# Optimization experiments

Measured on AMD Instinct MI355X. Metric: run time of the kernel, lower is better.

The kernel has to match this reference:

```python
import jax, jax.numpy as jnp
import numpy as np

N = 50000      # nodes
E = 800000     # edges (avg degree 16)
F_IN = 128     # input feature dim
HID = 64       # hidden_channels
HEADS = 4
OUT = 64       # out_channels


def _gatv2_layer(x, src, dst, Wl, Wr, att, bias, heads, ch, n):
    # lin_l (source) and lin_r (target) projections -> [N, H, C]
    xl = (x @ Wl).reshape(n, heads, ch)
    xr = (x @ Wr).reshape(n, heads, ch)
    # per-edge GATv2 attention logits: a^T LeakyReLU(xl_j + xr_i)
    e = jax.nn.leaky_relu(xl[src] + xr[dst], negative_slope=0.2)  # [E, H, C]
    score = jnp.einsum('ehc,hc->eh', e, att)                      # [E, H]
    # segment softmax over incoming edges of each destination node
    m = jax.ops.segment_max(score, dst, num_segments=n)           # [N, H]
    m = jnp.where(jnp.isfinite(m), m, 0.0)
    p = jnp.exp(score - m[dst])
    denom = jax.ops.segment_sum(p, dst, num_segments=n)           # [N, H]
    alpha = p / (denom[dst] + 1e-16)                              # [E, H]
    # weighted scatter-aggregate of source messages xl_j
    out = jax.ops.segment_sum(alpha[..., None] * xl[src], dst, num_segments=n)
    return out.reshape(n, heads * ch) + bias


def setup_inputs() -> dict:
    key = jax.random.key(0)
    ks = jax.random.split(key, 16)

    def w(k, shape, fan_in):
        return (jax.random.normal(k, shape, dtype=jnp.float32) / np.sqrt(fan_in)).astype(jnp.float32)

    return {
        'x': jax.random.normal(ks[0], (N, F_IN), dtype=jnp.float32),
        'Wl1': w(ks[1], (F_IN, HEADS * HID), F_IN),
        'Wr1': w(ks[2], (F_IN, HEADS * HID), F_IN),
        'att1': w(ks[3], (HEADS, HID), HID),
        'b1': jnp.zeros((HEADS * HID,), jnp.float32),
        'Wl2': w(ks[4], (HEADS * HID, HEADS * HID), HEADS * HID),
        'Wr2': w(ks[5], (HEADS * HID, HEADS * HID), HEADS * HID),
        'att2': w(ks[6], (HEADS, HID), HID),
        'b2': jnp.zeros((HEADS * HID,), jnp.float32),
        'Wl3': w(ks[7], (HEADS * HID, OUT), HEADS * HID),
        'Wr3': w(ks[8], (HEADS * HID, OUT), HEADS * HID),
        'att3': w(ks[9], (1, OUT), OUT),
        'b3': jnp.zeros((OUT,), jnp.float32),
        'Wlin': w(ks[10], (OUT, HID), OUT),
        'blin': jnp.zeros((HID,), jnp.float32),
        'edge_index': jax.random.randint(ks[11], (2, E), 0, N, dtype=jnp.int64
                                         if jax.config.read('jax_enable_x64') else jnp.int32),
    }


def reference(x, Wl1, Wr1, att1, b1, Wl2, Wr2, att2, b2, Wl3, Wr3, att3, b3, Wlin, blin, edge_index):
    src, dst = edge_index[0], edge_index[1]
    h = jax.nn.elu(_gatv2_layer(x, src, dst, Wl1, Wr1, att1, b1, HEADS, HID, N))
    h = jax.nn.elu(_gatv2_layer(h, src, dst, Wl2, Wr2, att2, b2, HEADS, HID, N))
    h = _gatv2_layer(h, src, dst, Wl3, Wr3, att3, b3, 1, OUT, N)
    # F.dropout(p=0.5, training=False) -> identity in eval mode
    return h @ Wlin + blin
```

## Files before the change

kernel.cpp:

```cpp
#include <hip/hip_runtime.h>
#include <hip/hip_fp16.h>

#define NN 50000
#define EE 800000

typedef float f32x4 __attribute__((ext_vector_type(4)));
typedef _Float16 f16x8 __attribute__((ext_vector_type(8)));
typedef _Float16 f16x4 __attribute__((ext_vector_type(4)));
typedef _Float16 f16x2 __attribute__((ext_vector_type(2)));

__global__ void hist_kernel(const int* __restrict__ dst, int* __restrict__ counts, int E) {
    int idx = blockIdx.x * blockDim.x + threadIdx.x;
    int stride = gridDim.x * blockDim.x;
    for (int e = idx; e < E; e += stride)
        atomicAdd(&counts[dst[e]], 1);
}

__global__ void scan_phaseA(const int* __restrict__ counts, int* __restrict__ bsum, int n) {
    __shared__ int buf[256];
    int b = blockIdx.x, t = threadIdx.x;
    int i = b * 256 + t;
    buf[t] = (i < n) ? counts[i] : 0;
    __syncthreads();
#pragma unroll
    for (int off = 128; off; off >>= 1) {
        if (t < off) buf[t] += buf[t + off];
        __syncthreads();
    }
    if (t == 0) bsum[b] = buf[0];
}

__global__ void scan_phaseB(int* __restrict__ bsum, int* __restrict__ row_off_n, int nb) {
    __shared__ int buf[256];
    int t = threadIdx.x;
    int v = (t < nb) ? bsum[t] : 0;
    buf[t] = v;
    __syncthreads();
#pragma unroll
    for (int off = 1; off < 256; off <<= 1) {
        int x = (t >= off) ? buf[t - off] : 0;
        __syncthreads();
        buf[t] += x;
        __syncthreads();
    }
    if (t < nb) bsum[t] = buf[t] - v;
    if (t == 255) *row_off_n = buf[255];
}

__global__ void scan_phaseC(const int* __restrict__ counts, const int* __restrict__ bsum,
                            int* __restrict__ row_off, int n) {
    __shared__ int buf[256];
    int b = blockIdx.x, t = threadIdx.x;
    int i = b * 256 + t;
    int v = (i < n) ? counts[i] : 0;
    buf[t] = v;
    __syncthreads();
#pragma unroll
    for (int off = 1; off < 256; off <<= 1) {
        int x = (t >= off) ? buf[t - off] : 0;
        __syncthreads();
        buf[t] += x;
        __syncthreads();
    }
    if (i < n) row_off[i] = bsum[b] + buf[t] - v;
}

__global__ void scatter_kernel(const int* __restrict__ src, const int* __restrict__ dst,
                               const int* __restrict__ row_off, int* __restrict__ cursor,
                               int* __restrict__ esrc, int E) {
    int idx = blockIdx.x * blockDim.x + threadIdx.x;
    int stride = gridDim.x * blockDim.x;
    for (int e = idx; e < E; e += stride) {
        int d = dst[e];
        int pos = row_off[d] + atomicAdd(&cursor[d], 1);
        esrc[pos] = src[e];
    }
}

__device__ __forceinline__ void wfrag_store(__half* o, int K, int col, int k, float v) {
    int KS = K >> 5;
    int cgni = col >> 4, l15 = col & 15;
    int ks = k >> 5, qq = (k >> 3) & 3, ee = k & 7;
    size_t flat = ((size_t)(cgni * KS + ks) * 64 + qq * 16 + l15) * 8 + ee;
    o[flat] = __float2half_rn(v);
}

__global__ void prep_all(const float* __restrict__ Wl1, const float* __restrict__ Wr1,
                         const float* __restrict__ Wl2, const float* __restrict__ Wr2,
                         const float* __restrict__ Wl3, const float* __restrict__ Wr3,
                         const float* __restrict__ Wlin,
                         __half* __restrict__ w1, __half* __restrict__ w2,
                         __half* __restrict__ w3, __half* __restrict__ w4,
                         const float* __restrict__ x, __half* __restrict__ xf, int n4x) {
    int idx = blockIdx.x * blockDim.x + threadIdx.x;
    if (idx < 233472) {
        const float* W; __half* o; int K, Nc, roff, li;
        if (idx < 65536) {
            K = 128; Nc = 256; o = w1;
            if (idx < 32768) { W = Wl1; li = idx; roff = 0; }
            else             { W = Wr1; li = idx - 32768; roff = 256; }
        } else if (idx < 196608) {
            K = 256; Nc = 256; o = w2;
            if (idx < 131072) { W = Wl2; li = idx - 65536; roff = 0; }
            else              { W = Wr2; li = idx - 131072; roff = 256; }
        } else if (idx < 229376) {
            K = 256; Nc = 64; o = w3;
            if (idx < 212992) { W = Wl3; li = idx - 196608; roff = 0; }
            else              { W = Wr3; li = idx - 212992; roff = 64; }
        } else {
            K = 64; Nc = 64; o = w4; W = Wlin; li = idx - 229376; roff = 0;
        }
        int k = li / Nc, n = li - k * Nc;
        wfrag_store(o, K, roff + n, k, W[li]);
    } else {
        int xi = idx - 233472;
        if (xi < n4x) {
            float4 v = *(const float4*)(x + (size_t)xi * 4);
            f16x4 h = {(_Float16)v.x, (_Float16)v.y, (_Float16)v.z, (_Float16)v.w};
            *(f16x4*)((_Float16*)xf + (size_t)xi * 4) = h;
        }
    }
}

template <int KS, int COLG>
__global__ __launch_bounds__(COLG * 256) void gemm_ws(
        const __half* __restrict__ A, const __half* __restrict__ Bt,
        int M, int nTiles, int Nc, int splitCol,
        __half* __restrict__ outL, __half* __restrict__ outR,
        float* __restrict__ outF, const float* __restrict__ bias) {
    constexpr int K = KS * 32;
    int tid = threadIdx.x;
    int lane = tid & 63;
    int w = tid >> 6;
    int rs = w & 3;
    int cg = w >> 2;
    int l15 = lane & 15, q = lane >> 4;
    int colbase = blockIdx.y * (COLG * 64) + cg * 64;

    const _Float16* Ap = (const _Float16*)A;
    const f16x8* Bf = (const f16x8*)Bt;
    int cgni0 = (blockIdx.y * COLG + cg) * 4;

    f16x8 bfrag[KS][4];
#pragma unroll
    for (int ks = 0; ks < KS; ++ks)
#pragma unroll
        for (int ni = 0; ni < 4; ++ni)
            bfrag[ks][ni] = Bf[((size_t)(cgni0 + ni) * KS + ks) * 64 + lane];

    int tile = blockIdx.x;
    if (tile >= nTiles) return;

    f16x8 afrag[KS];
    {
        int row = tile * 64 + rs * 16 + l15;
        if (row >= M) row = M - 1;
        const _Float16* ap = Ap + (size_t)row * K + q * 8;
#pragma unroll
        for (int ks = 0; ks < KS; ++ks) afrag[ks] = *(const f16x8*)(ap + ks * 32);
    }

    while (true) {
        int next = tile + gridDim.x;
        bool has = (next < nTiles);
        f16x8 anext[KS];
        if (has) {
            int row = next * 64 + rs * 16 + l15;
            if (row >= M) row = M - 1;
            const _Float16* ap = Ap + (size_t)row * K + q * 8;
#pragma unroll
            for (int ks = 0; ks < KS; ++ks) anext[ks] = *(const f16x8*)(ap + ks * 32);
        }

        f32x4 acc[4] = {};
#pragma unroll
        for (int ks = 0; ks < KS; ++ks)
#pragma unroll
            for (int ni = 0; ni < 4; ++ni)
                acc[ni] = __builtin_amdgcn_mfma_f32_16x16x32_f16(afrag[ks], bfrag[ks][ni], acc[ni], 0, 0, 0);

#pragma unroll
        for (int ni = 0; ni < 4; ++ni) {
            int gc = colbase + ni * 16 + l15;
            if (outF) {
                float bv = bias ? bias[gc] : 0.f;
#pragma unroll
                for (int r = 0; r < 4; ++r) {
                    int gr = tile * 64 + rs * 16 + q * 4 + r;
                    if (gr < M) outF[(size_t)gr * Nc + gc] = acc[ni][r] + bv;
                }
            } else {
                __half* dp = outL; int cc = gc;
                if (gc >= splitCol) { dp = outR; cc = gc - splitCol; }
#pragma unroll
                for (int r = 0; r < 4; ++r) {
                    int gr = tile * 64 + rs * 16 + q * 4 + r;
                    if (gr < M) dp[(size_t)gr * splitCol + cc] = __float2half_rn(acc[ni][r]);
                }
            }
        }
        if (!has) break;
#pragma unroll
        for (int ks = 0; ks < KS; ++ks) afrag[ks] = anext[ks];
        tile = next;
    }
}

template <int CTRL>
__device__ __forceinline__ float dpp_add_f32(float x) {
    int y = __builtin_amdgcn_mov_dpp(__float_as_int(x), CTRL, 0xF, 0xF, true);
    return x + __int_as_float(y);
}

__global__ __launch_bounds__(256, 4) void gat_gather_h4(
        const __half* __restrict__ xl, const __half* __restrict__ xr,
        const float* __restrict__ att, const float* __restrict__ bias,
        const int* __restrict__ row_off, const int* __restrict__ esrc,
        __half* __restrict__ out, int n) {
    const float LOG2E = 1.44269504f;
    int wave = threadIdx.x >> 6;
    int lane = threadIdx.x & 63;
    int node = blockIdx.x * 4 + wave;
    if (node >= n) return;
    int eslot = lane >> 4;
    unsigned j = lane & 15;

    const uint4* xl16 = (const uint4*)xl;
    unsigned jo = 2u * j;

    f16x2 xrv[8];
    *(uint4*)(&xrv[0]) = ((const uint4*)xr)[((unsigned)node << 5) + jo];
    *(uint4*)(&xrv[4]) = ((const uint4*)xr)[((unsigned)node << 5) + jo + 1];

    float4 a0 = *(const float4*)(att + j * 16);
    float4 a1 = *(const float4*)(att + j * 16 + 4);
    float4 a2 = *(const float4*)(att + j * 16 + 8);
    float4 a3 = *(const float4*)(att + j * 16 + 12);
    f16x2 atv[8] = {
        {(_Float16)(a0.x * LOG2E), (_Float16)(a0.y * LOG2E)},
        {(_Float16)(a0.z * LOG2E), (_Float16)(a0.w * LOG2E)},
        {(_Float16)(a1.x * LOG2E), (_Float16)(a1.y * LOG2E)},
        {(_Float16)(a1.z * LOG2E), (_Float16)(a1.w * LOG2E)},
        {(_Float16)(a2.x * LOG2E), (_Float16)(a2.y * LOG2E)},
        {(_Float16)(a2.z * LOG2E), (_Float16)(a2.w * LOG2E)},
        {(_Float16)(a3.x * LOG2E), (_Float16)(a3.y * LOG2E)},
        {(_Float16)(a3.z * LOG2E), (_Float16)(a3.w * LOG2E)}};
    const f16x2 k02 = {(_Float16)0.2f, (_Float16)0.2f};

    float acc[16] = {};
    float L = 0.f;

    int e0 = row_off[node], e1 = row_off[node + 1];
    int elast = (e1 > e0) ? e1 - 1 : 0;

    int sA = esrc[min(e0 + 0 + eslot, elast)];
    int sB = esrc[min(e0 + 4 + eslot, elast)];
    int sC = esrc[min(e0 + 8 + eslot, elast)];
    uint4 A0 = xl16[((unsigned)sA << 5) + jo], A1 = xl16[((unsigned)sA << 5) + jo + 1];
    uint4 B0 = xl16[((unsigned)sB << 5) + jo], B1 = xl16[((unsigned)sB << 5) + jo + 1];
    uint4 C0 = xl16[((unsigned)sC << 5) + jo], C1 = xl16[((unsigned)sC << 5) + jo + 1];

#define H4_PHASE(R0, R1, EB)                                                  \
    {                                                                         \
        f16x2 v[8];                                                           \
        *(uint4*)(&v[0]) = R0;                                                \
        *(uint4*)(&v[4]) = R1;                                                \
        float t0 = 0.f, t1 = 0.f;                                             \
        _Pragma("unroll")                                                     \
        for (int k = 0; k < 4; ++k) {                                         \
            f16x2 sa = v[k] + xrv[k];                                         \
            f16x2 ra = __builtin_elementwise_max(sa, sa * k02);               \
            t0 = __builtin_amdgcn_fdot2(ra, atv[k], t0, false);               \
            f16x2 sb = v[k + 4] + xrv[k + 4];                                 \
            f16x2 rb = __builtin_elementwise_max(sb, sb * k02);               \
            t1 = __builtin_amdgcn_fdot2(rb, atv[k + 4], t1, false);           \
        }                                                                     \
        float t = t0 + t1;                                                    \
        t = dpp_add_f32<0xB1>(t);                                             \
        t = dpp_add_f32<0x4E>(t);                                             \
        float p = exp2f(t);                                                   \
        p = ((EB) + eslot < e1) ? p : 0.f;                                    \
        L += p;                                                               \
        _Pragma("unroll")                                                     \
        for (int k = 0; k < 8; ++k) {                                         \
            acc[2 * k]     = fmaf((float)v[k].x, p, acc[2 * k]);              \
            acc[2 * k + 1] = fmaf((float)v[k].y, p, acc[2 * k + 1]);          \
        }                                                                     \
    }

    for (int e = e0; e < e1; e += 12) {
        int nsA = esrc[min(e + 12 + eslot, elast)];
        int nsB = esrc[min(e + 16 + eslot, elast)];
        int nsC = esrc[min(e + 20 + eslot, elast)];
        H4_PHASE(A0, A1, e)
        A0 = xl16[((unsigned)nsA << 5) + jo];
        A1 = xl16[((unsigned)nsA << 5) + jo + 1];
        H4_PHASE(B0, B1, e + 4)
        B0 = xl16[((unsigned)nsB << 5) + jo];
        B1 = xl16[((unsigned)nsB << 5) + jo + 1];
        H4_PHASE(C0, C1, e + 8)
        C0 = xl16[((unsigned)nsC << 5) + jo];
        C1 = xl16[((unsigned)nsC << 5) + jo + 1];
    }
#undef H4_PHASE

#pragma unroll
    for (int k = 0; k < 16; ++k) {
        acc[k] += __shfl_xor(acc[k], 16);
        acc[k] += __shfl_xor(acc[k], 32);
    }
    L += __shfl_xor(L, 16);
    L += __shfl_xor(L, 32);

    if (eslot == 0) {
        float inv = 1.f / (L + 1e-16f);
        float4 b0 = *(const float4*)(bias + j * 16);
        float4 b1v = *(const float4*)(bias + j * 16 + 4);
        float4 b2v = *(const float4*)(bias + j * 16 + 8);
        float4 b3v = *(const float4*)(bias + j * 16 + 12);
        float bb[16] = {b0.x,  b0.y,  b0.z,  b0.w,  b1v.x, b1v.y, b1v.z, b1v.w,
                        b2v.x, b2v.y, b2v.z, b2v.w, b3v.x, b3v.y, b3v.z, b3v.w};
        f16x8 o0, o1;
#pragma unroll
        for (int k = 0; k < 8; ++k) {
            float vA = acc[k] * inv + bb[k];
            vA = vA > 0.f ? vA : __expf(vA) - 1.f;
            o0[k] = (_Float16)vA;
            float vB = acc[k + 8] * inv + bb[k + 8];
            vB = vB > 0.f ? vB : __expf(vB) - 1.f;
            o1[k] = (_Float16)vB;
        }
        _Float16* op = (_Float16*)out + ((size_t)node << 8) + j * 16;
        *(f16x8*)op = o0;
        *(f16x8*)(op + 8) = o1;
    }
}

__global__ __launch_bounds__(256, 4) void gat_gather_h1(
        const __half* __restrict__ xl, const __half* __restrict__ xr,
        const float* __restrict__ att, const float* __restrict__ bias,
        const int* __restrict__ row_off, const int* __restrict__ esrc,
        __half* __restrict__ out, int n) {
    const float LOG2E = 1.44269504f;
    int wave = threadIdx.x >> 6;
    int lane = threadIdx.x & 63;
    int node = blockIdx.x * 4 + wave;
    if (node >= n) return;
    int eslot = lane >> 3;
    unsigned j = lane & 7;

    const uint4* xl16 = (const uint4*)xl;

    f16x2 xrv[4];
    *(uint4*)(&xrv[0]) = ((const uint4*)xr)[((unsigned)node << 3) + j];

    float4 a0 = *(const float4*)(att + j * 8);
    float4 a1 = *(const float4*)(att + j * 8 + 4);
    f16x2 atv[4] = {
        {(_Float16)(a0.x * LOG2E), (_Float16)(a0.y * LOG2E)},
        {(_Float16)(a0.z * LOG2E), (_Float16)(a0.w * LOG2E)},
        {(_Float16)(a1.x * LOG2E), (_Float16)(a1.y * LOG2E)},
        {(_Float16)(a1.z * LOG2E), (_Float16)(a1.w * LOG2E)}};
    const f16x2 k02 = {(_Float16)0.2f, (_Float16)0.2f};

    float acc[8] = {};
    float L = 0.f;

    int e0 = row_off[node], e1 = row_off[node + 1];
    int elast = (e1 > e0) ? e1 - 1 : 0;

    int sA = esrc[min(e0 +  0 + eslot, elast)];
    int sB = esrc[min(e0 +  8 + eslot, elast)];
    int sC = esrc[min(e0 + 16 + eslot, elast)];
    uint4 A = xl16[((unsigned)sA << 3) + j];
    uint4 B = xl16[((unsigned)sB << 3) + j];
    uint4 C = xl16[((unsigned)sC << 3) + j];

#define H1_PHASE(R, EB)                                                       \
    {                                                                         \
        f16x2 v[4];                                                           \
        *(uint4*)(&v[0]) = R;                                                 \
        float t0 = 0.f, t1 = 0.f;                                             \
        {                                                                     \
            f16x2 s0 = v[0] + xrv[0];                                         \
            f16x2 r0 = __builtin_elementwise_max(s0, s0 * k02);               \
            t0 = __builtin_amdgcn_fdot2(r0, atv[0], t0, false);               \
            f16x2 s1 = v[1] + xrv[1];                                         \
            f16x2 r1 = __builtin_elementwise_max(s1, s1 * k02);               \
            t0 = __builtin_amdgcn_fdot2(r1, atv[1], t0, false);               \
            f16x2 s2 = v[2] + xrv[2];                                         \
            f16x2 r2 = __builtin_elementwise_max(s2, s2 * k02);               \
            t1 = __builtin_amdgcn_fdot2(r2, atv[2], t1, false);               \
            f16x2 s3 = v[3] + xrv[3];                                         \
            f16x2 r3 = __builtin_elementwise_max(s3, s3 * k02);               \
            t1 = __builtin_amdgcn_fdot2(r3, atv[3], t1, false);               \
        }                                                                     \
        float t = t0 + t1;                                                    \
        t = dpp_add_f32<0xB1>(t);                                             \
        t = dpp_add_f32<0x4E>(t);                                             \
        t = dpp_add_f32<0x141>(t);                                            \
        float p = exp2f(t);                                                   \
        p = ((EB) + eslot < e1) ? p : 0.f;                                    \
        L += p;                                                               \
        _Pragma("unroll")                                                     \
        for (int k = 0; k < 4; ++k) {                                         \
            acc[2 * k]     = fmaf((float)v[k].x, p, acc[2 * k]);              \
            acc[2 * k + 1] = fmaf((float)v[k].y, p, acc[2 * k + 1]);          \
        }                                                                     \
    }

    for (int e = e0; e < e1; e += 24) {
        int nsA = esrc[min(e + 24 + eslot, elast)];
        int nsB = esrc[min(e + 32 + eslot, elast)];
        int nsC = esrc[min(e + 40 + eslot, elast)];
        H1_PHASE(A, e)
        A = xl16[((unsigned)nsA << 3) + j];
        H1_PHASE(B, e + 8)
        B = xl16[((unsigned)nsB << 3) + j];
        H1_PHASE(C, e + 16)
        C = xl16[((unsigned)nsC << 3) + j];
    }
#undef H1_PHASE

#pragma unroll
    for (int k = 0; k < 8; ++k) {
        acc[k] += __shfl_xor(acc[k], 8);
        acc[k] += __shfl_xor(acc[k], 16);
        acc[k] += __shfl_xor(acc[k], 32);
    }
    L += __shfl_xor(L, 8);
    L += __shfl_xor(L, 16);
    L += __shfl_xor(L, 32);

    if (eslot == 0) {
        float inv = 1.f / (L + 1e-16f);
        float4 b0 = *(const float4*)(bias + j * 8);
        float4 b1v = *(const float4*)(bias + j * 8 + 4);
        float bb[8] = {b0.x, b0.y, b0.z, b0.w, b1v.x, b1v.y, b1v.z, b1v.w};
        f16x8 ov;
#pragma unroll
        for (int k = 0; k < 8; ++k)
            ov[k] = (_Float16)(acc[k] * inv + bb[k]);
        *(f16x8*)((_Float16*)out + ((size_t)node << 6) + j * 8) = ov;
    }
}

extern "C" void kernel_launch(void* const* d_in, const int* in_sizes, int n_in,
                              void* d_out, int out_size, void* d_ws, size_t ws_size,
                              hipStream_t stream) {
    const float* x    = (const float*)d_in[0];
    const float* Wl1  = (const float*)d_in[1];
    const float* Wr1  = (const float*)d_in[2];
    const float* att1 = (const float*)d_in[3];
    const float* b1   = (const float*)d_in[4];
    const float* Wl2  = (const float*)d_in[5];
    const float* Wr2  = (const float*)d_in[6];
    const float* att2 = (const float*)d_in[7];
    const float* b2   = (const float*)d_in[8];
    const float* Wl3  = (const float*)d_in[9];
    const float* Wr3  = (const float*)d_in[10];
    const float* att3 = (const float*)d_in[11];
    const float* b3   = (const float*)d_in[12];
    const float* Wlin = (const float*)d_in[13];
    const float* blin = (const float*)d_in[14];
    const int*   ei   = (const int*)d_in[15];
    const int* src = ei;
    const int* dst = ei + EE;

    const int N = NN, E = EE;
    const int NB = (N + 255) / 256;

    __half* xf = (__half*)d_ws;
    __half* xl = xf + (size_t)N * 128;
    __half* xr = xl + (size_t)N * 256;
    __half* H  = xr + (size_t)N * 256;
    __half* G  = H + (size_t)N * 256;
    __half* w1 = G + (size_t)N * 64;
    __half* w2 = w1 + 65536;
    __half* w3 = w2 + 131072;
    __half* w4 = w3 + 32768;
    int* row_off = (int*)(w4 + 4096);
    int* tmp     = row_off + (N + 1);
    int* esrc    = tmp + 2 * N;
    int* bsum    = esrc + E;

    hipMemsetAsync(tmp, 0, (size_t)2 * N * sizeof(int), stream);
    hist_kernel<<<1024, 256, 0, stream>>>(dst, tmp, E);
    scan_phaseA<<<NB, 256, 0, stream>>>(tmp, bsum, N);
    scan_phaseB<<<1, 256, 0, stream>>>(bsum, row_off + N, NB);
    scan_phaseC<<<NB, 256, 0, stream>>>(tmp, bsum, row_off, N);
    scatter_kernel<<<1024, 256, 0, stream>>>(src, dst, row_off, tmp + N, esrc, E);

    int n4x = N * 128 / 4;
    prep_all<<<(233472 + n4x + 255) / 256, 256, 0, stream>>>(
        Wl1, Wr1, Wl2, Wr2, Wl3, Wr3, Wlin, w1, w2, w3, w4, x, xf, n4x);

    int nTiles = (N + 63) / 64;
    int gatherBlocks = (N + 3) / 4;

    gemm_ws<4, 2><<<dim3(128, 4), 512, 0, stream>>>(
        xf, w1, N, nTiles, 512, 256, xl, xr, nullptr, nullptr);
    gat_gather_h4<<<gatherBlocks, 256, 0, stream>>>(xl, xr, att1, b1, row_off, esrc, H, N);

    gemm_ws<8, 2><<<dim3(128, 4), 512, 0, stream>>>(
        H, w2, N, nTiles, 512, 256, xl, xr, nullptr, nullptr);
    gat_gather_h4<<<gatherBlocks, 256, 0, stream>>>(xl, xr, att2, b2, row_off, esrc, H, N);

    gemm_ws<8, 2><<<dim3(256, 1), 512, 0, stream>>>(
        H, w3, N, nTiles, 128, 64, xl, xr, nullptr, nullptr);
    gat_gather_h1<<<gatherBlocks, 256, 0, stream>>>(xl, xr, att3, b3, row_off, esrc, G, N);

    gemm_ws<2, 1><<<dim3(512, 1), 256, 0, stream>>>(
        G, w4, N, nTiles, 64, 64, nullptr, nullptr, (float*)d_out, blin);
}
```

Baseline: 477.5 us.

## Remap 4-head gather to 32 lanes per edge with finer-grained early-exit loops

The 4-head gather kernel now gives each edge 32 lanes holding 8 channels each, processing 2 edges per wave step instead of 4 edges with 16 channels per lane. This halves the per-lane accumulator and register footprint, and the launch bound is raised to 8 blocks per CU to allow more resident waves. Both gather kernels switch from fixed multi-phase iterations to loops that exit after each phase, cutting masked wasted work on low-degree nodes. The trade-offs are an extra DPP reduction step per edge and more serial phases per node.

```diff
diff --git a/kernel.cpp b/kernel.cpp
--- a/kernel.cpp
+++ b/kernel.cpp
@@ -212,7 +212,7 @@
     return x + __int_as_float(y);
 }
 
-__global__ __launch_bounds__(256, 4) void gat_gather_h4(
+__global__ __launch_bounds__(256, 8) void gat_gather_h4(
         const __half* __restrict__ xl, const __half* __restrict__ xr,
         const float* __restrict__ att, const float* __restrict__ bias,
         const int* __restrict__ row_off, const int* __restrict__ esrc,
@@ -222,121 +222,106 @@
     int lane = threadIdx.x & 63;
     int node = blockIdx.x * 4 + wave;
     if (node >= n) return;
-    int eslot = lane >> 4;
-    unsigned j = lane & 15;
+    int slot = lane >> 5;
+    unsigned jj = lane & 31;
 
     const uint4* xl16 = (const uint4*)xl;
-    unsigned jo = 2u * j;
-
-    f16x2 xrv[8];
-    *(uint4*)(&xrv[0]) = ((const uint4*)xr)[((unsigned)node << 5) + jo];
-    *(uint4*)(&xrv[4]) = ((const uint4*)xr)[((unsigned)node << 5) + jo + 1];
-
-    float4 a0 = *(const float4*)(att + j * 16);
-    float4 a1 = *(const float4*)(att + j * 16 + 4);
-    float4 a2 = *(const float4*)(att + j * 16 + 8);
-    float4 a3 = *(const float4*)(att + j * 16 + 12);
-    f16x2 atv[8] = {
+
+    f16x2 xrv[4];
+    *(uint4*)(&xrv[0]) = ((const uint4*)xr)[((unsigned)node << 5) + jj];
+
+    float4 a0 = *(const float4*)(att + jj * 8);
+    float4 a1 = *(const float4*)(att + jj * 8 + 4);
+    f16x2 atv[4] = {
         {(_Float16)(a0.x * LOG2E), (_Float16)(a0.y * LOG2E)},
         {(_Float16)(a0.z * LOG2E), (_Float16)(a0.w * LOG2E)},
         {(_Float16)(a1.x * LOG2E), (_Float16)(a1.y * LOG2E)},
-        {(_Float16)(a1.z * LOG2E), (_Float16)(a1.w * LOG2E)},
-        {(_Float16)(a2.x * LOG2E), (_Float16)(a2.y * LOG2E)},
-        {(_Float16)(a2.z * LOG2E), (_Float16)(a2.w * LOG2E)},
-        {(_Float16)(a3.x * LOG2E), (_Float16)(a3.y * LOG2E)},
-        {(_Float16)(a3.z * LOG2E), (_Float16)(a3.w * LOG2E)}};
+        {(_Float16)(a1.z * LOG2E), (_Float16)(a1.w * LOG2E)}};
     const f16x2 k02 = {(_Float16)0.2f, (_Float16)0.2f};
 
-    float acc[16] = {};
+    float acc[8] = {};
     float L = 0.f;
 
     int e0 = row_off[node], e1 = row_off[node + 1];
     int elast = (e1 > e0) ? e1 - 1 : 0;
 
-    int sA = esrc[min(e0 + 0 + eslot, elast)];
-    int sB = esrc[min(e0 + 4 + eslot, elast)];
-    int sC = esrc[min(e0 + 8 + eslot, elast)];
-    uint4 A0 = xl16[((unsigned)sA << 5) + jo], A1 = xl16[((unsigned)sA << 5) + jo + 1];
-    uint4 B0 = xl16[((unsigned)sB << 5) + jo], B1 = xl16[((unsigned)sB << 5) + jo + 1];
-    uint4 C0 = xl16[((unsigned)sC << 5) + jo], C1 = xl16[((unsigned)sC << 5) + jo + 1];
-
-#define H4_PHASE(R0, R1, EB)                                                  \
+    int sA = esrc[min(e0 + 0 + slot, elast)];
+    int sB = esrc[min(e0 + 2 + slot, elast)];
+    int sC = esrc[min(e0 + 4 + slot, elast)];
+    int sD = esrc[min(e0 + 6 + slot, elast)];
+    uint4 A = xl16[((unsigned)sA << 5) + jj];
+    uint4 B = xl16[((unsigned)sB << 5) + jj];
+    uint4 C = xl16[((unsigned)sC << 5) + jj];
+    uint4 D = xl16[((unsigned)sD << 5) + jj];
+
+#define H4_PHASE(BUF, EB)                                                     \
     {                                                                         \
-        f16x2 v[8];                                                           \
-        *(uint4*)(&v[0]) = R0;                                                \
-        *(uint4*)(&v[4]) = R1;                                                \
-        float t0 = 0.f, t1 = 0.f;                                             \
+        f16x2 v[4];                                                           \
+        *(uint4*)(&v[0]) = BUF;                                               \
+        float t = 0.f;                                                        \
         _Pragma("unroll")                                                     \
         for (int k = 0; k < 4; ++k) {                                         \
-            f16x2 sa = v[k] + xrv[k];                                         \
-            f16x2 ra = __builtin_elementwise_max(sa, sa * k02);               \
-            t0 = __builtin_amdgcn_fdot2(ra, atv[k], t0, false);               \
-            f16x2 sb = v[k + 4] + xrv[k + 4];                                 \
-            f16x2 rb = __builtin_elementwise_max(sb, sb * k02);               \
-            t1 = __builtin_amdgcn_fdot2(rb, atv[k + 4], t1, false);           \
+            f16x2 s = v[k] + xrv[k];                                          \
+            f16x2 r = __builtin_elementwise_max(s, s * k02);                  \
+            t = __builtin_amdgcn_fdot2(r, atv[k], t, false);                  \
         }                                                                     \
-        float t = t0 + t1;                                                    \
         t = dpp_add_f32<0xB1>(t);                                             \
         t = dpp_add_f32<0x4E>(t);                                             \
+        t = dpp_add_f32<0x141>(t);                                            \
         float p = exp2f(t);                                                   \
-        p = ((EB) + eslot < e1) ? p : 0.f;                                    \
+        p = ((EB) + slot < e1) ? p : 0.f;                                     \
         L += p;                                                               \
         _Pragma("unroll")                                                     \
-        for (int k = 0; k < 8; ++k) {                                         \
+        for (int k = 0; k < 4; ++k) {                                         \
             acc[2 * k]     = fmaf((float)v[k].x, p, acc[2 * k]);              \
             acc[2 * k + 1] = fmaf((float)v[k].y, p, acc[2 * k + 1]);          \
         }                                                                     \
     }
 
-    for (int e = e0; e < e1; e += 12) {
-        int nsA = esrc[min(e + 12 + eslot, elast)];
-        int nsB = esrc[min(e + 16 + eslot, elast)];
-        int nsC = esrc[min(e + 20 + eslot, elast)];
-        H4_PHASE(A0, A1, e)
-        A0 = xl16[((unsigned)nsA << 5) + jo];
-        A1 = xl16[((unsigned)nsA << 5) + jo + 1];
-        H4_PHASE(B0, B1, e + 4)
-        B0 = xl16[((unsigned)nsB << 5) + jo];
-        B1 = xl16[((unsigned)nsB << 5) + jo + 1];
-        H4_PHASE(C0, C1, e + 8)
-        C0 = xl16[((unsigned)nsC << 5) + jo];
-        C1 = xl16[((unsigned)nsC << 5) + jo + 1];
+    {
+        int e = e0;
+        while (true) {
+            int ns = esrc[min(e + 8 + slot, elast)];
+            H4_PHASE(A, e)
+            A = xl16[((unsigned)ns << 5) + jj];
+            e += 2; if (e >= e1) break;
+            ns = esrc[min(e + 8 + slot, elast)];
+            H4_PHASE(B, e)
+            B = xl16[((unsigned)ns << 5) + jj];
+            e += 2; if (e >= e1) break;
+            ns = esrc[min(e + 8 + slot, elast)];
+            H4_PHASE(C, e)
+            C = xl16[((unsigned)ns << 5) + jj];
+            e += 2; if (e >= e1) break;
+            ns = esrc[min(e + 8 + slot, elast)];
+            H4_PHASE(D, e)
+            D = xl16[((unsigned)ns << 5) + jj];
+            e += 2; if (e >= e1) break;
+        }
     }
 #undef H4_PHASE
 
 #pragma unroll
-    for (int k = 0; k < 16; ++k) {
-        acc[k] += __shfl_xor(acc[k], 16);
-        acc[k] += __shfl_xor(acc[k], 32);
-    }
-    L += __shfl_xor(L, 16);
+    for (int k = 0; k < 8; ++k) acc[k] += __shfl_xor(acc[k], 32);
     L += __shfl_xor(L, 32);
 
-    if (eslot == 0) {
+    if (slot == 0) {
         float inv = 1.f / (L + 1e-16f);
-        float4 b0 = *(const float4*)(bias + j * 16);
-        float4 b1v = *(const float4*)(bias + j * 16 + 4);
-        float4 b2v = *(const float4*)(bias + j * 16 + 8);
-        float4 b3v = *(const float4*)(bias + j * 16 + 12);
-        float bb[16] = {b0.x,  b0.y,  b0.z,  b0.w,  b1v.x, b1v.y, b1v.z, b1v.w,
-                        b2v.x, b2v.y, b2v.z, b2v.w, b3v.x, b3v.y, b3v.z, b3v.w};
-        f16x8 o0, o1;
+        float4 b0 = *(const float4*)(bias + jj * 8);
+        float4 b1v = *(const float4*)(bias + jj * 8 + 4);
+        float bb[8] = {b0.x, b0.y, b0.z, b0.w, b1v.x, b1v.y, b1v.z, b1v.w};
+        f16x8 o0;
 #pragma unroll
         for (int k = 0; k < 8; ++k) {
             float vA = acc[k] * inv + bb[k];
             vA = vA > 0.f ? vA : __expf(vA) - 1.f;
             o0[k] = (_Float16)vA;
-            float vB = acc[k + 8] * inv + bb[k + 8];
-            vB = vB > 0.f ? vB : __expf(vB) - 1.f;
-            o1[k] = (_Float16)vB;
-        }
-        _Float16* op = (_Float16*)out + ((size_t)node << 8) + j * 16;
-        *(f16x8*)op = o0;
-        *(f16x8*)(op + 8) = o1;
-    }
-}
-
-__global__ __launch_bounds__(256, 4) void gat_gather_h1(
+        }
+        *(f16x8*)((_Float16*)out + ((size_t)node << 8) + jj * 8) = o0;
+    }
+}
+
+__global__ __launch_bounds__(256, 8) void gat_gather_h1(
         const __half* __restrict__ xl, const __half* __restrict__ xr,
         const float* __restrict__ att, const float* __restrict__ bias,
         const int* __restrict__ row_off, const int* __restrict__ esrc,
@@ -409,16 +394,22 @@
         }                                                                     \
     }
 
-    for (int e = e0; e < e1; e += 24) {
-        int nsA = esrc[min(e + 24 + eslot, elast)];
-        int nsB = esrc[min(e + 32 + eslot, elast)];
-        int nsC = esrc[min(e + 40 + eslot, elast)];
-        H1_PHASE(A, e)
-        A = xl16[((unsigned)nsA << 3) + j];
-        H1_PHASE(B, e + 8)
-        B = xl16[((unsigned)nsB << 3) + j];
-        H1_PHASE(C, e + 16)
-        C = xl16[((unsigned)nsC << 3) + j];
+    {
+        int e = e0;
+        while (true) {
+            int ns = esrc[min(e + 24 + eslot, elast)];
+            H1_PHASE(A, e)
+            A = xl16[((unsigned)ns << 3) + j];
+            e += 8; if (e >= e1) break;
+            ns = esrc[min(e + 24 + eslot, elast)];
+            H1_PHASE(B, e)
+            B = xl16[((unsigned)ns << 3) + j];
+            e += 8; if (e >= e1) break;
+            ns = esrc[min(e + 24 + eslot, elast)];
+            H1_PHASE(C, e)
+            C = xl16[((unsigned)ns << 3) + j];
+            e += 8; if (e >= e1) break;
+        }
     }
 #undef H1_PHASE
 
```

Result: faster. 463.1 us (-3.0%).
